# Kernel tuning notes

Hardware: AMD Instinct MI355X
Metric: run time of the kernel (lower is better)

## Reference

```python
import jax, jax.numpy as jnp
import numpy as np

B, T, N = 2, 512, 512
H = 64          # hidden_dim
S = 8           # static_dim
C = 8           # coord_dim
DYN = 4         # dynamic feature dim (hard-coded in module)
SELF_LOOP_W = 1.0


def setup_inputs() -> dict:
    key = jax.random.key(0)
    ks = jax.random.split(key, 12)
    x = jax.random.normal(ks[0], (B, T, N), dtype=jnp.float32)
    mask = jax.random.randint(ks[1], (B, T, N), 0, 2).astype(jnp.float32)
    static_context = jax.random.normal(ks[2], (N, S), dtype=jnp.float32)
    node_coords = jax.random.normal(ks[3], (N, C), dtype=jnp.float32)
    sc = 0.1
    W1 = jax.random.normal(ks[4], (DYN + S, H), dtype=jnp.float32) * sc
    b1 = jnp.zeros((H,), dtype=jnp.float32)
    W2 = jax.random.normal(ks[5], (H, H), dtype=jnp.float32) * sc
    b2 = jnp.zeros((H,), dtype=jnp.float32)
    W3 = jax.random.normal(ks[6], (4 * H, H), dtype=jnp.float32) * sc
    b3 = jnp.zeros((H,), dtype=jnp.float32)
    W4 = jax.random.normal(ks[7], (H, 1), dtype=jnp.float32) * sc
    b4 = jnp.zeros((1,), dtype=jnp.float32)
    return {"x": x, "mask": mask, "static_context": static_context,
            "node_coords": node_coords, "W1": W1, "b1": b1, "W2": W2,
            "b2": b2, "W3": W3, "b3": b3, "W4": W4, "b4": b4}


def _dynamic_context(x, mask):
    observed = 1.0 - mask                                  # (B,T,N)
    count = jnp.maximum(observed.sum(axis=1), 1.0)          # (B,N)
    mean = (x * observed).sum(axis=1) / count               # (B,N)
    centered = (x - mean[:, None, :]) * observed
    std = jnp.sqrt((centered ** 2).sum(axis=1) / count + 1e-6)
    # last observed value per node
    t_idx = jnp.arange(x.shape[1], dtype=x.dtype)[None, :, None]
    latest = jnp.argmax(t_idx * observed, axis=1)           # (B,N) int
    last = jnp.take_along_axis(x, latest[:, None, :], axis=1)[:, 0, :]
    missing_ratio = mask.mean(axis=1)                       # (B,N)
    return jnp.stack([mean, std, last, missing_ratio], axis=-1)  # (B,N,4)


def _prior_adjacency(node_coords):
    diff = node_coords[:, None, :] - node_coords[None, :, :]  # (N,N,C)
    d2 = (diff ** 2).sum(-1)
    dist = jnp.where(d2 > 0, jnp.sqrt(jnp.where(d2 > 0, d2, 1.0)), 0.0)
    prior = 1.0 / (1.0 + dist)
    eye = jnp.eye(node_coords.shape[0], dtype=node_coords.dtype)
    return prior * (1.0 - eye)


def reference(x, mask, static_context, node_coords, W1, b1, W2, b2, W3, b3, W4, b4):
    batch = x.shape[0]
    node_dynamic = _dynamic_context(x, mask)                         # (B,N,4)
    node_static = jnp.broadcast_to(static_context[None], (batch,) + static_context.shape)
    feats = jnp.concatenate([node_dynamic, node_static], axis=-1)    # (B,N,4+S)
    h = jax.nn.relu(feats @ W1 + b1)
    node_repr = jax.nn.relu(h @ W2 + b2)                              # (B,N,H)

    h_i = node_repr[:, :, None, :]                                    # (B,N,1,H)
    h_j = node_repr[:, None, :, :]                                    # (B,1,N,H)
    hi = jnp.broadcast_to(h_i, (batch, N, N, H))
    hj = jnp.broadcast_to(h_j, (batch, N, N, H))
    pair = jnp.concatenate([hi, hj, jnp.abs(hi - hj), hi * hj], axis=-1)  # (B,N,N,4H)
    e = jax.nn.relu(pair @ W3 + b3)
    edge_mod = jax.nn.relu((e @ W4 + b4)[..., 0])                     # (B,N,N)

    prior = _prior_adjacency(node_coords)[None]                       # (1,N,N)
    eye = jnp.eye(N, dtype=x.dtype)[None]
    adapt = edge_mod * prior + eye * SELF_LOOP_W
    degree = jnp.maximum(adapt.sum(axis=-1), 1e-6)                    # (B,N)
    inv_sqrt = degree ** -0.5
    return inv_sqrt[:, :, None] * adapt * inv_sqrt[:, None, :]
```

## Files before the change

### kernel.cpp

```cpp
#include <hip/hip_runtime.h>
#include <math.h>

#define B_ 2
#define T_ 512
#define N_ 512
#define H_ 64

typedef _Float16 half8 __attribute__((ext_vector_type(8)));
typedef __attribute__((ext_vector_type(4))) float floatx4;

__device__ inline half8 habs8(half8 v) {
    union { half8 h; unsigned u[4]; } x; x.h = v;
    x.u[0] &= 0x7fff7fffu; x.u[1] &= 0x7fff7fffu;
    x.u[2] &= 0x7fff7fffu; x.u[3] &= 0x7fff7fffu;
    return x.h;
}

__global__ void prep_kernel(const float* __restrict__ x, const float* __restrict__ mask,
                            const float* __restrict__ W3,
                            float* __restrict__ part, _Float16* __restrict__ W3ph) {
    int blk = blockIdx.x;
    if (blk < 512) {
        int b  = blk >> 8;
        int nc = (blk >> 5) & 7;
        int tc = blk & 31;
        int tn = threadIdx.x & 63;
        int tt = threadIdx.x >> 6;
        int n  = nc * 64 + tn;

        float sx = 0.f, sxx = 0.f, cnt = 0.f, msum = 0.f, bv = 0.f, bt = -1.f;
#pragma unroll
        for (int it = 0; it < 4; it++) {
            int t = tc * 16 + it * 4 + tt;
            int off = (b * T_ + t) * N_ + n;
            float xv = x[off];
            float mv = mask[off];
            float obs = 1.f - mv;
            sx   += xv * obs;
            sxx  += xv * xv * obs;
            cnt  += obs;
            msum += mv;
            if (obs > 0.5f) { bt = (float)t; bv = xv; }
        }

        __shared__ float red[6][4][64];
        red[0][tt][tn] = sx;  red[1][tt][tn] = sxx; red[2][tt][tn] = cnt;
        red[3][tt][tn] = msum; red[4][tt][tn] = bv; red[5][tt][tn] = bt;
        __syncthreads();

        if (threadIdx.x < 64) {
            float Sx = 0.f, Sxx = 0.f, Cnt = 0.f, Ms = 0.f, Bv = 0.f, Bt = -1.f;
#pragma unroll
            for (int u = 0; u < 4; u++) {
                Sx  += red[0][u][tn];
                Sxx += red[1][u][tn];
                Cnt += red[2][u][tn];
                Ms  += red[3][u][tn];
                float btu = red[5][u][tn];
                if (btu > Bt) { Bt = btu; Bv = red[4][u][tn]; }
            }
            const int plane = B_ * 32 * N_;
            int base = (b * 32 + tc) * N_ + n;
            part[0 * plane + base] = Sx;
            part[1 * plane + base] = Sxx;
            part[2 * plane + base] = Cnt;
            part[3 * plane + base] = Ms;
            part[4 * plane + base] = Bv;
            part[5 * plane + base] = Bt;
        }
    } else {
        int k = (blk - 512) * 256 + threadIdx.x;
        int t = k & 7;
        int l = (k >> 3) & 63;
        int f = k >> 9;
        int s = f >> 2, nt = f & 3;
        int quad = l >> 4, col = l & 15;
        W3ph[k] = (_Float16)W3[(128 + s * 32 + quad * 8 + t) * H_ + nt * 16 + col];
    }
}

__global__ __launch_bounds__(64) void node_kernel(
        const float* __restrict__ part, const float* __restrict__ x,
        const float* __restrict__ sc,
        const float* __restrict__ W1, const float* __restrict__ b1,
        const float* __restrict__ W2, const float* __restrict__ b2,
        const float* __restrict__ W3,
        _Float16* __restrict__ nrh, float* __restrict__ P, float* __restrict__ Qp) {
    int blk = blockIdx.x;
    int b = blk >> 9;
    int n = blk & (N_ - 1);
    int o = threadIdx.x;

    __shared__ float f[12];
    __shared__ float h[H_];
    __shared__ float r[H_];

    {
        const int plane = B_ * 32 * N_;
        float Sx = 0.f, Sxx = 0.f, Cnt = 0.f, Ms = 0.f, Bv = 0.f, Bt = -1.f;
        if (o < 32) {
            int base = (b * 32 + o) * N_ + n;
            Sx  = part[0 * plane + base];
            Sxx = part[1 * plane + base];
            Cnt = part[2 * plane + base];
            Ms  = part[3 * plane + base];
            Bv  = part[4 * plane + base];
            Bt  = part[5 * plane + base];
        }
#pragma unroll
        for (int off = 1; off < 32; off <<= 1) {
            Sx  += __shfl_xor(Sx, off);
            Sxx += __shfl_xor(Sxx, off);
            Cnt += __shfl_xor(Cnt, off);
            Ms  += __shfl_xor(Ms, off);
            float obt = __shfl_xor(Bt, off);
            float obv = __shfl_xor(Bv, off);
            if (obt > Bt) { Bt = obt; Bv = obv; }
        }
        if (o == 0) {
            float count = fmaxf(Cnt, 1.f);
            float mean  = Sx / count;
            float var   = (Sxx - 2.f * mean * Sx + mean * mean * Cnt) / count;
            float stdv  = sqrtf(fmaxf(var, 0.f) + 1e-6f);
            float last  = (Bt >= 0.f) ? Bv : x[b * T_ * N_ + n];
            f[0] = mean; f[1] = stdv; f[2] = last; f[3] = Ms * (1.f / (float)T_);
        }
        if (o >= 4 && o < 12) f[o] = sc[n * 8 + (o - 4)];
    }
    __syncthreads();

    float a = b1[o];
#pragma unroll
    for (int k = 0; k < 12; k++) a += f[k] * W1[k * H_ + o];
    h[o] = fmaxf(a, 0.f);
    __syncthreads();

    float a2 = b2[o];
#pragma unroll 8
    for (int k = 0; k < H_; k++) a2 += h[k] * W2[k * H_ + o];
    float rv = fmaxf(a2, 0.f);
    r[o] = rv;
    nrh[(b * N_ + n) * H_ + o] = (_Float16)rv;
    __syncthreads();

    float p = 0.f, q = 0.f;
#pragma unroll 8
    for (int k = 0; k < H_; k++) {
        float rk = r[k];
        p += rk * W3[k * H_ + o];
        q += rk * W3[(H_ + k) * H_ + o];
    }
    P[(b * N_ + n) * H_ + o] = p;
    Qp[(b * N_ + n) * H_ + (o & 15) * 4 + (o >> 4)] = q;
}

__global__ __launch_bounds__(256) void pair_mfma_kernel(
        const _Float16* __restrict__ nrh, const float* __restrict__ P,
        const float* __restrict__ Qp, const _Float16* __restrict__ W3ph,
        const float* __restrict__ coords,
        const float* __restrict__ b3, const float* __restrict__ W4,
        const float* __restrict__ b4,
        float* __restrict__ adapt, float* __restrict__ degree) {
    int i = blockIdx.x;
    int tid = threadIdx.x;
    int w = tid >> 6;
    int l = tid & 63;
    int col = l & 15;
    int quad = l >> 4;

    __shared__ float sPrior[N_];
    __shared__ float sRow[B_][4];

    {
        float ci[8];
#pragma unroll
        for (int c = 0; c < 8; c++) ci[c] = coords[i * 8 + c];
        for (int jj = tid; jj < N_; jj += 256) {
            float d2 = 0.f;
#pragma unroll
            for (int c = 0; c < 8; c++) {
                float df = ci[c] - coords[jj * 8 + c];
                d2 += df * df;
            }
            float dist = (d2 > 0.f) ? sqrtf(d2) : 0.f;
            sPrior[jj] = (jj == i) ? 0.f : 1.f / (1.f + dist);
        }
    }

    half8 bf[4][4];
#pragma unroll
    for (int s = 0; s < 4; s++)
#pragma unroll
        for (int nt = 0; nt < 4; nt++)
            bf[s][nt] = *(const half8*)(W3ph + (((s * 4 + nt) * 64 + l) << 3));

    float b3v[4], w4v[4];
#pragma unroll
    for (int nt = 0; nt < 4; nt++) {
        int o = nt * 16 + col;
        b3v[nt] = b3[o];
        w4v[nt] = W4[o];
    }
    float b4s = b4[0];
    __syncthreads();

#pragma unroll 1
    for (int rb = 0; rb < B_; rb++) {
        const _Float16* hi_row = nrh + (rb * N_ + i) * H_;
        half8 hiA = *(const half8*)(hi_row + quad * 8);
        half8 hiB = *(const half8*)(hi_row + 32 + quad * 8);

        float pb3[4];
#pragma unroll
        for (int nt = 0; nt < 4; nt++)
            pb3[nt] = P[(rb * N_ + i) * H_ + nt * 16 + col] + b3v[nt];

        const _Float16* nrb = nrh + (rb * N_) * H_;
        float rsum = 0.f;

        half8 hA, hB;
        {
            const _Float16* p0 = nrb + (w * 128 + col) * H_;
            hA = *(const half8*)(p0 + quad * 8);
            hB = *(const half8*)(p0 + 32 + quad * 8);
        }

#pragma unroll
        for (int mt = 0; mt < 8; mt++) {
            int j0 = w * 128 + mt * 16;

            half8 nA, nB;
            if (mt < 7) {
                const _Float16* pn = nrb + (j0 + 16 + col) * H_;
                nA = *(const half8*)(pn + quad * 8);
                nB = *(const half8*)(pn + 32 + quad * 8);
            }

            floatx4 pv = *(const floatx4*)(sPrior + j0 + quad * 4);
            floatx4 qv[4];
#pragma unroll
            for (int r = 0; r < 4; r++)
                qv[r] = *(const floatx4*)(Qp + (rb * N_ + j0 + quad * 4 + r) * H_ + col * 4);

            half8 dA = habs8(hiA - hA);
            half8 dB = habs8(hiB - hB);
            half8 mA = hiA * hA;
            half8 mB = hiB * hB;

            floatx4 acc[4];
#pragma unroll
            for (int nt = 0; nt < 4; nt++) acc[nt] = (floatx4){0.f, 0.f, 0.f, 0.f};
#pragma unroll
            for (int nt = 0; nt < 4; nt++) {
                acc[nt] = __builtin_amdgcn_mfma_f32_16x16x32_f16(dA, bf[0][nt], acc[nt], 0, 0, 0);
                acc[nt] = __builtin_amdgcn_mfma_f32_16x16x32_f16(dB, bf[1][nt], acc[nt], 0, 0, 0);
                acc[nt] = __builtin_amdgcn_mfma_f32_16x16x32_f16(mA, bf[2][nt], acc[nt], 0, 0, 0);
                acc[nt] = __builtin_amdgcn_mfma_f32_16x16x32_f16(mB, bf[3][nt], acc[nt], 0, 0, 0);
            }

            float ed[4];
#pragma unroll
            for (int r = 0; r < 4; r++) {
                int j = j0 + quad * 4 + r;
                float p = 0.f;
#pragma unroll
                for (int nt = 0; nt < 4; nt++)
                    p += fmaxf(acc[nt][r] + pb3[nt] + qv[r][nt], 0.f) * w4v[nt];
                p += __shfl_xor(p, 1);
                p += __shfl_xor(p, 2);
                p += __shfl_xor(p, 4);
                p += __shfl_xor(p, 8);
                float edge = fmaxf(p + b4s, 0.f);
                float ad = (j == i) ? 1.0f : edge * pv[r];
                ed[r] = ad;
                rsum += ad;
            }
            if (col == 0) {
                *(floatx4*)&adapt[(size_t)(rb * N_ + i) * N_ + j0 + quad * 4] =
                    (floatx4){ed[0], ed[1], ed[2], ed[3]};
            }
            if (mt < 7) { hA = nA; hB = nB; }
        }

        rsum += __shfl_xor(rsum, 16);
        rsum += __shfl_xor(rsum, 32);
        if (l == 0) sRow[rb][w] = rsum;
    }

    __syncthreads();
    if (tid < B_)
        degree[tid * N_ + i] = sRow[tid][0] + sRow[tid][1] + sRow[tid][2] + sRow[tid][3];
}

__global__ void norm_kernel(const float* __restrict__ adapt, const float* __restrict__ deg,
                            float* __restrict__ out) {
    int idx = blockIdx.x * 256 + threadIdx.x;
    int b = idx >> 16;
    int r = (idx >> 7) & (N_ - 1);
    int c4 = (idx & 127) << 2;
    float dr = rsqrtf(fmaxf(deg[b * N_ + r], 1e-6f));
    floatx4 a = *(const floatx4*)(adapt + ((size_t)idx << 2));
    floatx4 o;
#pragma unroll
    for (int k = 0; k < 4; k++)
        o[k] = dr * a[k] * rsqrtf(fmaxf(deg[b * N_ + c4 + k], 1e-6f));
    *(floatx4*)(out + ((size_t)idx << 2)) = o;
}

extern "C" void kernel_launch(void* const* d_in, const int* in_sizes, int n_in,
                              void* d_out, int out_size, void* d_ws, size_t ws_size,
                              hipStream_t stream) {
    const float* x      = (const float*)d_in[0];
    const float* mask   = (const float*)d_in[1];
    const float* sc     = (const float*)d_in[2];
    const float* coords = (const float*)d_in[3];
    const float* W1 = (const float*)d_in[4];
    const float* b1 = (const float*)d_in[5];
    const float* W2 = (const float*)d_in[6];
    const float* b2 = (const float*)d_in[7];
    const float* W3 = (const float*)d_in[8];
    const float* b3 = (const float*)d_in[9];
    const float* W4 = (const float*)d_in[10];
    const float* b4 = (const float*)d_in[11];
    float* out = (float*)d_out;

    float* wsp = (float*)d_ws;
    float* P       = wsp;
    float* Qp      = wsp + 65536;
    _Float16* nrh  = (_Float16*)(wsp + 131072);
    _Float16* W3ph = (_Float16*)(wsp + 163840);
    float* deg     = wsp + 167936;
    float* adapt   = wsp + 168960;
    float* part    = adapt;

    prep_kernel<<<544, 256, 0, stream>>>(x, mask, W3, part, W3ph);
    node_kernel<<<B_ * N_, 64, 0, stream>>>(part, x, sc, W1, b1, W2, b2, W3, nrh, P, Qp);
    pair_mfma_kernel<<<N_, 256, 0, stream>>>(nrh, P, Qp, W3ph, coords, b3, W4, b4, adapt, deg);
    norm_kernel<<<512, 256, 0, stream>>>(adapt, deg, out);
}
```

Before: 109.6 us.

## Swap MFMA operands so each lane owns one pair column, simplifying epilogue reduction

Swaps the A/B operands of the MFMA so the accumulator is transposed: each lane now holds 16 hidden outputs for a single j column instead of 4 j rows. The epilogue then reduces across hidden units in registers with only two cross-lane shuffles per tile instead of four shuffles per row. P, b3, W4 and Q are loaded as float4 vectors in the matching layout, and Q is stored unpermuted. The trade-off is that adapt is written as scalar stores from 16 lanes instead of float4 stores, and the row-sum reduction shuffles change.

```diff
diff --git a/kernel.cpp b/kernel.cpp
--- a/kernel.cpp
+++ b/kernel.cpp
@@ -85,7 +85,7 @@
         const float* __restrict__ W1, const float* __restrict__ b1,
         const float* __restrict__ W2, const float* __restrict__ b2,
         const float* __restrict__ W3,
-        _Float16* __restrict__ nrh, float* __restrict__ P, float* __restrict__ Qp) {
+        _Float16* __restrict__ nrh, float* __restrict__ P, float* __restrict__ Q) {
     int blk = blockIdx.x;
     int b = blk >> 9;
     int n = blk & (N_ - 1);
@@ -151,12 +151,12 @@
         q += rk * W3[(H_ + k) * H_ + o];
     }
     P[(b * N_ + n) * H_ + o] = p;
-    Qp[(b * N_ + n) * H_ + (o & 15) * 4 + (o >> 4)] = q;
+    Q[(b * N_ + n) * H_ + o] = q;
 }
 
 __global__ __launch_bounds__(256) void pair_mfma_kernel(
         const _Float16* __restrict__ nrh, const float* __restrict__ P,
-        const float* __restrict__ Qp, const _Float16* __restrict__ W3ph,
+        const float* __restrict__ Q, const _Float16* __restrict__ W3ph,
         const float* __restrict__ coords,
         const float* __restrict__ b3, const float* __restrict__ W4,
         const float* __restrict__ b4,
@@ -194,12 +194,11 @@
         for (int nt = 0; nt < 4; nt++)
             bf[s][nt] = *(const half8*)(W3ph + (((s * 4 + nt) * 64 + l) << 3));
 
-    float b3v[4], w4v[4];
+    floatx4 w4s[4], b3s[4];
 #pragma unroll
     for (int nt = 0; nt < 4; nt++) {
-        int o = nt * 16 + col;
-        b3v[nt] = b3[o];
-        w4v[nt] = W4[o];
+        w4s[nt] = *(const floatx4*)(W4 + nt * 16 + quad * 4);
+        b3s[nt] = *(const floatx4*)(b3 + nt * 16 + quad * 4);
     }
     float b4s = b4[0];
     __syncthreads();
@@ -210,10 +209,10 @@
         half8 hiA = *(const half8*)(hi_row + quad * 8);
         half8 hiB = *(const half8*)(hi_row + 32 + quad * 8);
 
-        float pb3[4];
+        floatx4 spb[4];
 #pragma unroll
         for (int nt = 0; nt < 4; nt++)
-            pb3[nt] = P[(rb * N_ + i) * H_ + nt * 16 + col] + b3v[nt];
+            spb[nt] = *(const floatx4*)(P + (rb * N_ + i) * H_ + nt * 16 + quad * 4) + b3s[nt];
 
         const _Float16* nrb = nrh + (rb * N_) * H_;
         float rsum = 0.f;
@@ -228,6 +227,7 @@
 #pragma unroll
         for (int mt = 0; mt < 8; mt++) {
             int j0 = w * 128 + mt * 16;
+            int j = j0 + col;
 
             half8 nA, nB;
             if (mt < 7) {
@@ -236,11 +236,11 @@
                 nB = *(const half8*)(pn + 32 + quad * 8);
             }
 
-            floatx4 pv = *(const floatx4*)(sPrior + j0 + quad * 4);
+            float pr = sPrior[j];
             floatx4 qv[4];
 #pragma unroll
-            for (int r = 0; r < 4; r++)
-                qv[r] = *(const floatx4*)(Qp + (rb * N_ + j0 + quad * 4 + r) * H_ + col * 4);
+            for (int nt = 0; nt < 4; nt++)
+                qv[nt] = *(const floatx4*)(Q + (rb * N_ + j) * H_ + nt * 16 + quad * 4);
 
             half8 dA = habs8(hiA - hA);
             half8 dB = habs8(hiB - hB);
@@ -252,38 +252,35 @@
             for (int nt = 0; nt < 4; nt++) acc[nt] = (floatx4){0.f, 0.f, 0.f, 0.f};
 #pragma unroll
             for (int nt = 0; nt < 4; nt++) {
-                acc[nt] = __builtin_amdgcn_mfma_f32_16x16x32_f16(dA, bf[0][nt], acc[nt], 0, 0, 0);
-                acc[nt] = __builtin_amdgcn_mfma_f32_16x16x32_f16(dB, bf[1][nt], acc[nt], 0, 0, 0);
-                acc[nt] = __builtin_amdgcn_mfma_f32_16x16x32_f16(mA, bf[2][nt], acc[nt], 0, 0, 0);
-                acc[nt] = __builtin_amdgcn_mfma_f32_16x16x32_f16(mB, bf[3][nt], acc[nt], 0, 0, 0);
+                acc[nt] = __builtin_amdgcn_mfma_f32_16x16x32_f16(bf[0][nt], dA, acc[nt], 0, 0, 0);
+                acc[nt] = __builtin_amdgcn_mfma_f32_16x16x32_f16(bf[1][nt], dB, acc[nt], 0, 0, 0);
+                acc[nt] = __builtin_amdgcn_mfma_f32_16x16x32_f16(bf[2][nt], mA, acc[nt], 0, 0, 0);
+                acc[nt] = __builtin_amdgcn_mfma_f32_16x16x32_f16(bf[3][nt], mB, acc[nt], 0, 0, 0);
             }
 
-            float ed[4];
-#pragma unroll
-            for (int r = 0; r < 4; r++) {
-                int j = j0 + quad * 4 + r;
-                float p = 0.f;
-#pragma unroll
-                for (int nt = 0; nt < 4; nt++)
-                    p += fmaxf(acc[nt][r] + pb3[nt] + qv[r][nt], 0.f) * w4v[nt];
-                p += __shfl_xor(p, 1);
-                p += __shfl_xor(p, 2);
-                p += __shfl_xor(p, 4);
-                p += __shfl_xor(p, 8);
-                float edge = fmaxf(p + b4s, 0.f);
-                float ad = (j == i) ? 1.0f : edge * pv[r];
-                ed[r] = ad;
-                rsum += ad;
-            }
-            if (col == 0) {
-                *(floatx4*)&adapt[(size_t)(rb * N_ + i) * N_ + j0 + quad * 4] =
-                    (floatx4){ed[0], ed[1], ed[2], ed[3]};
-            }
+            float pe = 0.f;
+#pragma unroll
+            for (int nt = 0; nt < 4; nt++)
+#pragma unroll
+                for (int r = 0; r < 4; r++)
+                    pe += fmaxf(acc[nt][r] + spb[nt][r] + qv[nt][r], 0.f) * w4s[nt][r];
+
+            pe += __shfl_xor(pe, 16);
+            pe += __shfl_xor(pe, 32);
+
+            float edge = fmaxf(pe + b4s, 0.f);
+            float ad = (j == i) ? 1.0f : edge * pr;
+            if (quad == 0)
+                adapt[(size_t)(rb * N_ + i) * N_ + j] = ad;
+            rsum += ad;
+
             if (mt < 7) { hA = nA; hB = nB; }
         }
 
-        rsum += __shfl_xor(rsum, 16);
-        rsum += __shfl_xor(rsum, 32);
+        rsum += __shfl_xor(rsum, 1);
+        rsum += __shfl_xor(rsum, 2);
+        rsum += __shfl_xor(rsum, 4);
+        rsum += __shfl_xor(rsum, 8);
         if (l == 0) sRow[rb][w] = rsum;
     }
 
@@ -326,7 +323,7 @@
 
     float* wsp = (float*)d_ws;
     float* P       = wsp;
-    float* Qp      = wsp + 65536;
+    float* Q       = wsp + 65536;
     _Float16* nrh  = (_Float16*)(wsp + 131072);
     _Float16* W3ph = (_Float16*)(wsp + 163840);
     float* deg     = wsp + 167936;
@@ -334,7 +331,7 @@
     float* part    = adapt;
 
     prep_kernel<<<544, 256, 0, stream>>>(x, mask, W3, part, W3ph);
-    node_kernel<<<B_ * N_, 64, 0, stream>>>(part, x, sc, W1, b1, W2, b2, W3, nrh, P, Qp);
-    pair_mfma_kernel<<<N_, 256, 0, stream>>>(nrh, P, Qp, W3ph, coords, b3, W4, b4, adapt, deg);
+    node_kernel<<<B_ * N_, 64, 0, stream>>>(part, x, sc, W1, b1, W2, b2, W3, nrh, P, Q);
+    pair_mfma_kernel<<<N_, 256, 0, stream>>>(nrh, P, Q, W3ph, coords, b3, W4, b4, adapt, deg);
     norm_kernel<<<512, 256, 0, stream>>>(adapt, deg, out);
 }
```

Result: slower. 118.0 us (+7.7%).

## Process two rows i per block for one batch to reuse j-tile loads

Applied to the files above, without the earlier changes.

The pair kernel now gives each block two adjacent rows i0,i1 of a single batch instead of one row across both batches. Every loaded j-tile of node features and Qp values feeds two sets of MFMAs, roughly halving global loads per pair. The cost is computing the prior row twice per block and holding more registers, which may reduce occupancy.

```diff
diff --git a/kernel.cpp b/kernel.cpp
--- a/kernel.cpp
+++ b/kernel.cpp
@@ -161,20 +161,26 @@
         const float* __restrict__ b3, const float* __restrict__ W4,
         const float* __restrict__ b4,
         float* __restrict__ adapt, float* __restrict__ degree) {
-    int i = blockIdx.x;
+    int blk = blockIdx.x;
+    int rb = blk >> 8;
+    int ih = blk & 255;
+    int i0 = ih * 2;
+    int i1 = i0 + 1;
     int tid = threadIdx.x;
     int w = tid >> 6;
     int l = tid & 63;
     int col = l & 15;
     int quad = l >> 4;
 
-    __shared__ float sPrior[N_];
-    __shared__ float sRow[B_][4];
-
-    {
+    __shared__ __align__(16) float sPrior[2][N_];
+    __shared__ float sRow[2][4];
+
+#pragma unroll
+    for (int s = 0; s < 2; s++) {
+        int isel = i0 + s;
         float ci[8];
 #pragma unroll
-        for (int c = 0; c < 8; c++) ci[c] = coords[i * 8 + c];
+        for (int c = 0; c < 8; c++) ci[c] = coords[isel * 8 + c];
         for (int jj = tid; jj < N_; jj += 256) {
             float d2 = 0.f;
 #pragma unroll
@@ -183,7 +189,7 @@
                 d2 += df * df;
             }
             float dist = (d2 > 0.f) ? sqrtf(d2) : 0.f;
-            sPrior[jj] = (jj == i) ? 0.f : 1.f / (1.f + dist);
+            sPrior[s][jj] = (jj == isel) ? 0.f : 1.f / (1.f + dist);
         }
     }
 
@@ -194,58 +200,57 @@
         for (int nt = 0; nt < 4; nt++)
             bf[s][nt] = *(const half8*)(W3ph + (((s * 4 + nt) * 64 + l) << 3));
 
-    float b3v[4], w4v[4];
+    const _Float16* hi0_row = nrh + (rb * N_ + i0) * H_;
+    const _Float16* hi1_row = nrh + (rb * N_ + i1) * H_;
+    half8 hi0A = *(const half8*)(hi0_row + quad * 8);
+    half8 hi0B = *(const half8*)(hi0_row + 32 + quad * 8);
+    half8 hi1A = *(const half8*)(hi1_row + quad * 8);
+    half8 hi1B = *(const half8*)(hi1_row + 32 + quad * 8);
+
+    float pb30[4], pb31[4], w4v[4];
 #pragma unroll
     for (int nt = 0; nt < 4; nt++) {
         int o = nt * 16 + col;
-        b3v[nt] = b3[o];
+        float b3o = b3[o];
+        pb30[nt] = P[(rb * N_ + i0) * H_ + o] + b3o;
+        pb31[nt] = P[(rb * N_ + i1) * H_ + o] + b3o;
         w4v[nt] = W4[o];
     }
     float b4s = b4[0];
-    __syncthreads();
-
-#pragma unroll 1
-    for (int rb = 0; rb < B_; rb++) {
-        const _Float16* hi_row = nrh + (rb * N_ + i) * H_;
-        half8 hiA = *(const half8*)(hi_row + quad * 8);
-        half8 hiB = *(const half8*)(hi_row + 32 + quad * 8);
-
-        float pb3[4];
-#pragma unroll
-        for (int nt = 0; nt < 4; nt++)
-            pb3[nt] = P[(rb * N_ + i) * H_ + nt * 16 + col] + b3v[nt];
-
-        const _Float16* nrb = nrh + (rb * N_) * H_;
-        float rsum = 0.f;
-
-        half8 hA, hB;
+    const _Float16* nrb = nrh + (rb * N_) * H_;
+    float rsum0 = 0.f, rsum1 = 0.f;
+    __syncthreads();
+
+    half8 hA, hB;
+    {
+        const _Float16* p0 = nrb + (w * 128 + col) * H_;
+        hA = *(const half8*)(p0 + quad * 8);
+        hB = *(const half8*)(p0 + 32 + quad * 8);
+    }
+
+#pragma unroll
+    for (int mt = 0; mt < 8; mt++) {
+        int j0 = w * 128 + mt * 16;
+
+        half8 nA, nB;
+        if (mt < 7) {
+            const _Float16* pn = nrb + (j0 + 16 + col) * H_;
+            nA = *(const half8*)(pn + quad * 8);
+            nB = *(const half8*)(pn + 32 + quad * 8);
+        }
+
+        floatx4 pv0 = *(const floatx4*)(&sPrior[0][j0 + quad * 4]);
+        floatx4 pv1 = *(const floatx4*)(&sPrior[1][j0 + quad * 4]);
+        floatx4 qv[4];
+#pragma unroll
+        for (int r = 0; r < 4; r++)
+            qv[r] = *(const floatx4*)(Qp + (rb * N_ + j0 + quad * 4 + r) * H_ + col * 4);
+
         {
-            const _Float16* p0 = nrb + (w * 128 + col) * H_;
-            hA = *(const half8*)(p0 + quad * 8);
-            hB = *(const half8*)(p0 + 32 + quad * 8);
-        }
-
-#pragma unroll
-        for (int mt = 0; mt < 8; mt++) {
-            int j0 = w * 128 + mt * 16;
-
-            half8 nA, nB;
-            if (mt < 7) {
-                const _Float16* pn = nrb + (j0 + 16 + col) * H_;
-                nA = *(const half8*)(pn + quad * 8);
-                nB = *(const half8*)(pn + 32 + quad * 8);
-            }
-
-            floatx4 pv = *(const floatx4*)(sPrior + j0 + quad * 4);
-            floatx4 qv[4];
-#pragma unroll
-            for (int r = 0; r < 4; r++)
-                qv[r] = *(const floatx4*)(Qp + (rb * N_ + j0 + quad * 4 + r) * H_ + col * 4);
-
-            half8 dA = habs8(hiA - hA);
-            half8 dB = habs8(hiB - hB);
-            half8 mA = hiA * hA;
-            half8 mB = hiB * hB;
+            half8 dA = habs8(hi0A - hA);
+            half8 dB = habs8(hi0B - hB);
+            half8 mA = hi0A * hA;
+            half8 mB = hi0B * hB;
 
             floatx4 acc[4];
 #pragma unroll
@@ -265,31 +270,73 @@
                 float p = 0.f;
 #pragma unroll
                 for (int nt = 0; nt < 4; nt++)
-                    p += fmaxf(acc[nt][r] + pb3[nt] + qv[r][nt], 0.f) * w4v[nt];
+                    p += fmaxf(acc[nt][r] + pb30[nt] + qv[r][nt], 0.f) * w4v[nt];
                 p += __shfl_xor(p, 1);
                 p += __shfl_xor(p, 2);
                 p += __shfl_xor(p, 4);
                 p += __shfl_xor(p, 8);
                 float edge = fmaxf(p + b4s, 0.f);
-                float ad = (j == i) ? 1.0f : edge * pv[r];
+                float ad = (j == i0) ? 1.0f : edge * pv0[r];
                 ed[r] = ad;
-                rsum += ad;
+                rsum0 += ad;
             }
             if (col == 0) {
-                *(floatx4*)&adapt[(size_t)(rb * N_ + i) * N_ + j0 + quad * 4] =
+                *(floatx4*)&adapt[(size_t)(rb * N_ + i0) * N_ + j0 + quad * 4] =
                     (floatx4){ed[0], ed[1], ed[2], ed[3]};
             }
-            if (mt < 7) { hA = nA; hB = nB; }
-        }
-
-        rsum += __shfl_xor(rsum, 16);
-        rsum += __shfl_xor(rsum, 32);
-        if (l == 0) sRow[rb][w] = rsum;
-    }
-
-    __syncthreads();
-    if (tid < B_)
-        degree[tid * N_ + i] = sRow[tid][0] + sRow[tid][1] + sRow[tid][2] + sRow[tid][3];
+        }
+
+        {
+            half8 dA = habs8(hi1A - hA);
+            half8 dB = habs8(hi1B - hB);
+            half8 mA = hi1A * hA;
+            half8 mB = hi1B * hB;
+
+            floatx4 acc[4];
+#pragma unroll
+            for (int nt = 0; nt < 4; nt++) acc[nt] = (floatx4){0.f, 0.f, 0.f, 0.f};
+#pragma unroll
+            for (int nt = 0; nt < 4; nt++) {
+                acc[nt] = __builtin_amdgcn_mfma_f32_16x16x32_f16(dA, bf[0][nt], acc[nt], 0, 0, 0);
+                acc[nt] = __builtin_amdgcn_mfma_f32_16x16x32_f16(dB, bf[1][nt], acc[nt], 0, 0, 0);
+                acc[nt] = __builtin_amdgcn_mfma_f32_16x16x32_f16(mA, bf[2][nt], acc[nt], 0, 0, 0);
+                acc[nt] = __builtin_amdgcn_mfma_f32_16x16x32_f16(mB, bf[3][nt], acc[nt], 0, 0, 0);
+            }
+
+            float ed[4];
+#pragma unroll
+            for (int r = 0; r < 4; r++) {
+                int j = j0 + quad * 4 + r;
+                float p = 0.f;
+#pragma unroll
+                for (int nt = 0; nt < 4; nt++)
+                    p += fmaxf(acc[nt][r] + pb31[nt] + qv[r][nt], 0.f) * w4v[nt];
+                p += __shfl_xor(p, 1);
+                p += __shfl_xor(p, 2);
+                p += __shfl_xor(p, 4);
+                p += __shfl_xor(p, 8);
+                float edge = fmaxf(p + b4s, 0.f);
+                float ad = (j == i1) ? 1.0f : edge * pv1[r];
+                ed[r] = ad;
+                rsum1 += ad;
+            }
+            if (col == 0) {
+                *(floatx4*)&adapt[(size_t)(rb * N_ + i1) * N_ + j0 + quad * 4] =
+                    (floatx4){ed[0], ed[1], ed[2], ed[3]};
+            }
+        }
+
+        if (mt < 7) { hA = nA; hB = nB; }
+    }
+
+    rsum0 += __shfl_xor(rsum0, 16);
+    rsum0 += __shfl_xor(rsum0, 32);
+    rsum1 += __shfl_xor(rsum1, 16);
+    rsum1 += __shfl_xor(rsum1, 32);
+    if (l == 0) { sRow[0][w] = rsum0; sRow[1][w] = rsum1; }
+    __syncthreads();
+    if (tid < 2)
+        degree[rb * N_ + i0 + tid] = sRow[tid][0] + sRow[tid][1] + sRow[tid][2] + sRow[tid][3];
 }
 
 __global__ void norm_kernel(const float* __restrict__ adapt, const float* __restrict__ deg,
@@ -335,6 +382,6 @@
 
     prep_kernel<<<544, 256, 0, stream>>>(x, mask, W3, part, W3ph);
     node_kernel<<<B_ * N_, 64, 0, stream>>>(part, x, sc, W1, b1, W2, b2, W3, nrh, P, Qp);
-    pair_mfma_kernel<<<N_, 256, 0, stream>>>(nrh, P, Qp, W3ph, coords, b3, W4, b4, adapt, deg);
+    pair_mfma_kernel<<<512, 256, 0, stream>>>(nrh, P, Qp, W3ph, coords, b3, W4, b4, adapt, deg);
     norm_kernel<<<512, 256, 0, stream>>>(adapt, deg, out);
 }
```

Result: no change. 109.5 us (-0.1%).
